# Performance work log

Hardware: AMD Instinct MI355X
Metric: run time of the kernel (lower is better)

## Reference

```python
import jax, jax.numpy as jnp
import numpy as np

V, E, H, B, T = 50257, 300, 512, 4, 512  # vocab, embed(300 fixed), hid_size, batch, max_seq_len


def setup_inputs() -> dict:
    key = jax.random.key(0)
    ks = jax.random.split(key, 12)
    n = lambda k, shp, s: jax.random.normal(k, shp, dtype=jnp.float32) * s
    return {
        "tokens": jax.random.randint(ks[0], (B, T), 0, V),
        "emb_table": n(ks[1], (V, E), 0.02),      # frozen pretrained embedding
        # forward-direction LstmCellWithProjection params (cell_size == hidden_size == H)
        "W_ih_f": n(ks[2], (E, 4 * H), 0.05),     # input_linearity (no bias)
        "W_hh_f": n(ks[3], (H, 4 * H), 0.05),     # state_linearity weight
        "b_f": jnp.zeros((4 * H,), jnp.float32),  # state_linearity bias
        "W_proj_f": n(ks[4], (H, H), 0.05),       # state_projection (no bias)
        # backward direction
        "W_ih_b": n(ks[5], (E, 4 * H), 0.05),
        "W_hh_b": n(ks[6], (H, 4 * H), 0.05),
        "b_b": jnp.zeros((4 * H,), jnp.float32),
        "W_proj_b": n(ks[7], (H, H), 0.05),
        # final vocab projection nn.Linear(H, V)
        "W_lin": n(ks[8], (H, V), 0.02),
        "b_lin": jnp.zeros((V,), jnp.float32),
    }


def _lstm_proj_scan(x, W_ih, W_hh, b, W_proj):
    """ElmoLstm's LstmCellWithProjection over time. x: [B,T,E] -> [B,T,H]."""
    xp = jnp.einsum("bte,eg->btg", x, W_ih)  # precompute input projections [B,T,4H]

    def step(carry, xt):  # xt: [B,4H]
        h, c = carry
        p = xt + h @ W_hh + b
        i = jax.nn.sigmoid(p[:, :H])
        f = jax.nn.sigmoid(p[:, H:2 * H])
        g = jnp.tanh(p[:, 2 * H:3 * H])
        o = jax.nn.sigmoid(p[:, 3 * H:])
        c2 = i * g + f * c
        h2 = (o * jnp.tanh(c2)) @ W_proj  # projected hidden state
        return (h2, c2), h2

    init = (jnp.zeros((x.shape[0], H), x.dtype), jnp.zeros((x.shape[0], H), x.dtype))
    _, hs = jax.lax.scan(step, init, jnp.swapaxes(xp, 0, 1))  # [T,B,H]
    return jnp.swapaxes(hs, 0, 1)  # [B,T,H]


def reference(tokens, emb_table, W_ih_f, W_hh_f, b_f, W_proj_f,
              W_ih_b, W_hh_b, b_b, W_proj_b, W_lin, b_lin):
    x = emb_table[tokens]  # embedding gather [B,T,E]
    fwd = _lstm_proj_scan(x, W_ih_f, W_hh_f, b_f, W_proj_f)
    bwd = _lstm_proj_scan(x[:, ::-1], W_ih_b, W_hh_b, b_b, W_proj_b)[:, ::-1]
    # num_layers == 1 -> enc is (1,B,T,2H); fwd half / bwd half each through shared Linear
    logits_fwd = (fwd @ W_lin + b_lin).reshape(-1, V)  # [B*T, V]
    logits_bwd = (bwd @ W_lin + b_lin).reshape(-1, V)
    return jnp.concatenate([logits_fwd, logits_bwd], axis=0)  # [2*B*T, V]
```

## Files before the change

kernel.cpp:

```cpp
#include <hip/hip_runtime.h>
#include <hip/hip_bf16.h>

typedef unsigned short u16;
typedef unsigned int u32;
typedef unsigned long long u64;
typedef short bf16x8 __attribute__((ext_vector_type(8)));
typedef float f32x4 __attribute__((ext_vector_type(4)));

#define AS1C(p) ((const __attribute__((address_space(1))) void*)(p))
#define AS3(p)  ((__attribute__((address_space(3))) void*)(p))

__device__ __forceinline__ u16 f2bf(float f) {
    union { float f; unsigned u; } v; v.f = f;
    unsigned x = v.u;
    unsigned r = (x + 0x7FFFu + ((x >> 16) & 1u)) >> 16;
    return (u16)r;
}

__global__ void zero_init(u64* htag) {
    for (int i = threadIdx.x; i < 2 * 2 * 4 * 256; i += 256) htag[i] = 0ull;
}

__global__ void gather_emb(const int* __restrict__ tokens, const float* __restrict__ emb,
                           u16* __restrict__ xemb) {
    int row = blockIdx.x;
    int tok = tokens[row];
    const float* src = emb + (size_t)tok * 300;
    u16* dst = xemb + (size_t)row * 320;
    int c = threadIdx.x;
    if (c < 320) dst[c] = (c < 300) ? f2bf(src[c]) : (u16)0;
    c += 256;
    if (c < 320) dst[c] = (c < 300) ? f2bf(src[c]) : (u16)0;
}

__global__ void transpose_cvt(const float* __restrict__ in, u16* __restrict__ out,
                              int R, int C, int outR, int ldO) {
    __shared__ float tile[32][33];
    int c0 = blockIdx.x * 32, r0 = blockIdx.y * 32;
    int tx = threadIdx.x & 31, ty = threadIdx.x >> 5;
#pragma unroll
    for (int yy = 0; yy < 4; ++yy) {
        int r = r0 + ty + yy * 8, cc = c0 + tx;
        tile[ty + yy * 8][tx] = (r < R && cc < C) ? in[(size_t)r * C + cc] : 0.f;
    }
    __syncthreads();
#pragma unroll
    for (int yy = 0; yy < 4; ++yy) {
        int c = c0 + ty + yy * 8, r = r0 + tx;
        if (c < outR && r < ldO) out[(size_t)c * ldO + r] = f2bf(tile[tx][ty + yy * 8]);
    }
}

__global__ void cvt_flat(const float* __restrict__ in, u16* __restrict__ out, int n) {
    for (int i = blockIdx.x * 256 + threadIdx.x; i < n; i += gridDim.x * 256)
        out[i] = f2bf(in[i]);
}

__global__ __launch_bounds__(256) void gemm_bf16(
    const u16* __restrict__ A, const u16* __restrict__ BT,
    float* __restrict__ Cf, u16* __restrict__ Cb,
    const float* __restrict__ bias,
    int M, int Nreal, int K, int ldA, int ldB, int ldC,
    int arev, int orev, int orow_base)
{
    __shared__ char As[8192];
    __shared__ char Bs[8192];
    const int tid = threadIdx.x;
    const int lane = tid & 63;
    const int wid = tid >> 6;
    const int wr = wid >> 1, wc = wid & 1;
    const int m0 = blockIdx.y * 128;
    const int n0 = blockIdx.x * 128;

    f32x4 zero4 = {0.f, 0.f, 0.f, 0.f};
    f32x4 acc[4][4];
#pragma unroll
    for (int i = 0; i < 4; ++i)
#pragma unroll
        for (int j = 0; j < 4; ++j) acc[i][j] = zero4;

    const int kIters = K >> 5;
    const int l15 = lane & 15, kg = lane >> 4;

    const int srow0 = wid * 32 + (lane >> 2);
    const int srow1 = srow0 + 16;
    const int c0 = (lane & 3) ^ (srow0 & 3);
    const int c1 = (lane & 3) ^ (srow1 & 3);
    int ar0 = m0 + srow0, ar1 = m0 + srow1;
    if (arev) {
        ar0 = (ar0 & ~511) | (511 - (ar0 & 511));
        ar1 = (ar1 & ~511) | (511 - (ar1 & 511));
    }
    const u16* ga0 = A + (size_t)ar0 * ldA + c0 * 8;
    const u16* ga1 = A + (size_t)ar1 * ldA + c1 * 8;
    const u16* gb0 = BT + (size_t)(n0 + srow0) * ldB + c0 * 8;
    const u16* gb1 = BT + (size_t)(n0 + srow1) * ldB + c1 * 8;
    char* ldsA0 = As + wid * 2048;
    char* ldsA1 = As + wid * 2048 + 1024;
    char* ldsB0 = Bs + wid * 2048;
    char* ldsB1 = Bs + wid * 2048 + 1024;

    for (int kt = 0; kt < kIters; ++kt) {
        const int k0 = kt * 32;
        __builtin_amdgcn_global_load_lds(AS1C(ga0 + k0), AS3(ldsA0), 16, 0, 0);
        __builtin_amdgcn_global_load_lds(AS1C(ga1 + k0), AS3(ldsA1), 16, 0, 0);
        __builtin_amdgcn_global_load_lds(AS1C(gb0 + k0), AS3(ldsB0), 16, 0, 0);
        __builtin_amdgcn_global_load_lds(AS1C(gb1 + k0), AS3(ldsB1), 16, 0, 0);
        __syncthreads();

        bf16x8 af[4], bfr[4];
#pragma unroll
        for (int mt = 0; mt < 4; ++mt) {
            int r = wr * 64 + mt * 16 + l15;
            af[mt] = *(const bf16x8*)(As + r * 64 + ((kg ^ (r & 3)) * 16));
        }
#pragma unroll
        for (int nt = 0; nt < 4; ++nt) {
            int r = wc * 64 + nt * 16 + l15;
            bfr[nt] = *(const bf16x8*)(Bs + r * 64 + ((kg ^ (r & 3)) * 16));
        }
#pragma unroll
        for (int mt = 0; mt < 4; ++mt)
#pragma unroll
            for (int nt = 0; nt < 4; ++nt)
                acc[mt][nt] = __builtin_amdgcn_mfma_f32_16x16x32_bf16(af[mt], bfr[nt], acc[mt][nt], 0, 0, 0);
        __syncthreads();
    }

#pragma unroll
    for (int nt = 0; nt < 4; ++nt) {
        int col = n0 + wc * 64 + nt * 16 + l15;
        float bv = (bias != nullptr && col < Nreal) ? bias[col] : 0.f;
#pragma unroll
        for (int mt = 0; mt < 4; ++mt) {
#pragma unroll
            for (int j = 0; j < 4; ++j) {
                int m = m0 + wr * 64 + mt * 16 + kg * 4 + j;
                int om = orev ? ((m & ~511) | (511 - (m & 511))) : m;
                om += orow_base;
                if (col < Nreal) {
                    float v = acc[mt][nt][j] + bv;
                    if (Cf) Cf[(size_t)om * ldC + col] = v;
                    else    Cb[(size_t)om * ldC + col] = f2bf(v);
                }
            }
        }
    }
}

__global__ __launch_bounds__(256) void lstm_rec(
    const float* __restrict__ Wc_f, const float* __restrict__ Wc_b,
    const float* __restrict__ xp_f, const float* __restrict__ xp_b,
    u64* __restrict__ htag,
    u16* __restrict__ hpre_f, u16* __restrict__ hpre_b)
{
    __shared__ u16 hlds[4][520];
    __shared__ float gsum[4][4][16];
    __shared__ float cbuf[4][16];
    const int tid = threadIdx.x;
    const int dir = blockIdx.x >> 5;
    const int blk = blockIdx.x & 31;
    const int lane = tid & 63;
    const int wid = tid >> 6;
    const int l15 = lane & 15;
    const int kg = lane >> 4;

    const float* wcsrc = dir ? Wc_b : Wc_f;
    const float* xp    = dir ? xp_b : xp_f;
    u16* hpre          = dir ? hpre_b : hpre_f;
    u64* ht            = htag + (size_t)dir * 2 * 4 * 256;

    bf16x8 wcf[16];
#pragma unroll
    for (int ks = 0; ks < 16; ++ks) {
        bf16x8 w;
#pragma unroll
        for (int e = 0; e < 8; ++e) {
            int k = ks * 32 + kg * 8 + e;
            w[e] = (short)f2bf(wcsrc[(size_t)k * 2048 + wid * 512 + blk * 16 + l15]);
        }
        wcf[ks] = w;
    }
    if (tid < 64) cbuf[tid >> 4][tid & 15] = 0.f;
    __syncthreads();

    const bf16x8 zero8 = {0, 0, 0, 0, 0, 0, 0, 0};

    for (int t = 0; t < 512; ++t) {
        float xpv0 = 0.f, xpv1 = 0.f, xpv2 = 0.f, xpv3 = 0.f;
        const int b = tid >> 4, hu = tid & 15;
        if (tid < 64) {
            const float* xr = xp + ((size_t)(b * 512 + t)) * 2048 + blk * 16 + hu;
            xpv0 = xr[0]; xpv1 = xr[512]; xpv2 = xr[1024]; xpv3 = xr[1536];
        }
        {
            const u64* src = ht + (size_t)(t & 1) * 4 * 256;
            const u32 target = (u32)t;
            u64 w0, w1, w2, w3;
            for (;;) {
                w0 = __hip_atomic_load(&src[0 * 256 + tid], __ATOMIC_RELAXED, __HIP_MEMORY_SCOPE_AGENT);
                w1 = __hip_atomic_load(&src[1 * 256 + tid], __ATOMIC_RELAXED, __HIP_MEMORY_SCOPE_AGENT);
                w2 = __hip_atomic_load(&src[2 * 256 + tid], __ATOMIC_RELAXED, __HIP_MEMORY_SCOPE_AGENT);
                w3 = __hip_atomic_load(&src[3 * 256 + tid], __ATOMIC_RELAXED, __HIP_MEMORY_SCOPE_AGENT);
                if (((u32)(w0 >> 32) == target) & ((u32)(w1 >> 32) == target) &
                    ((u32)(w2 >> 32) == target) & ((u32)(w3 >> 32) == target)) break;
                __builtin_amdgcn_s_sleep(1);
            }
            asm volatile("" ::: "memory");
            *(u32*)&hlds[0][tid * 2] = (u32)w0;
            *(u32*)&hlds[1][tid * 2] = (u32)w1;
            *(u32*)&hlds[2][tid * 2] = (u32)w2;
            *(u32*)&hlds[3][tid * 2] = (u32)w3;
        }
        __syncthreads();

        f32x4 acc0 = {0.f, 0.f, 0.f, 0.f}, acc1 = {0.f, 0.f, 0.f, 0.f};
#pragma unroll
        for (int ks = 0; ks < 16; ++ks) {
            bf16x8 a = zero8;
            if (l15 < 4) a = *(const bf16x8*)&hlds[l15][ks * 32 + kg * 8];
            if (ks & 1) acc1 = __builtin_amdgcn_mfma_f32_16x16x32_bf16(a, wcf[ks], acc1, 0, 0, 0);
            else        acc0 = __builtin_amdgcn_mfma_f32_16x16x32_bf16(a, wcf[ks], acc0, 0, 0, 0);
        }
        f32x4 accs = acc0 + acc1;
        if (lane < 16) {
#pragma unroll
            for (int j = 0; j < 4; ++j) gsum[wid][j][lane] = accs[j];
        }
        __syncthreads();

        if (tid < 64) {
            float pi = xpv0 + gsum[0][b][hu];
            float pf = xpv1 + gsum[1][b][hu];
            float pg = xpv2 + gsum[2][b][hu];
            float po = xpv3 + gsum[3][b][hu];
            float iv = 1.f / (1.f + expf(-pi));
            float fv = 1.f / (1.f + expf(-pf));
            float gv = tanhf(pg);
            float ov = 1.f / (1.f + expf(-po));
            float c2 = iv * gv + fv * cbuf[b][hu];
            cbuf[b][hu] = c2;
            u16 hpb = f2bf(ov * tanhf(c2));
            hpre[(size_t)(b * 512 + t) * 512 + blk * 16 + hu] = hpb;
            unsigned v = hpb;
            unsigned nb = (unsigned)__shfl_down((int)v, 1);
            if ((tid & 1) == 0) {
                u32 packed = v | (nb << 16);
                u64 val = ((u64)(u32)(t + 1) << 32) | (u64)packed;
                size_t idx = (size_t)(((t + 1) & 1) * 4 + b) * 256 + blk * 8 + (hu >> 1);
                __hip_atomic_store(&ht[idx], val, __ATOMIC_RELAXED, __HIP_MEMORY_SCOPE_AGENT);
            }
        }
    }
}

extern "C" void kernel_launch(void* const* d_in, const int* in_sizes, int n_in,
                              void* d_out, int out_size, void* d_ws, size_t ws_size,
                              hipStream_t stream) {
    const int*   tokens   = (const int*)d_in[0];
    const float* emb      = (const float*)d_in[1];
    const float* W_ih_f   = (const float*)d_in[2];
    const float* W_hh_f   = (const float*)d_in[3];
    const float* b_f      = (const float*)d_in[4];
    const float* W_proj_f = (const float*)d_in[5];
    const float* W_ih_b   = (const float*)d_in[6];
    const float* W_hh_b   = (const float*)d_in[7];
    const float* b_b      = (const float*)d_in[8];
    const float* W_proj_b = (const float*)d_in[9];
    const float* W_lin    = (const float*)d_in[10];
    const float* b_lin    = (const float*)d_in[11];
    float* out = (float*)d_out;

    char* ws = (char*)d_ws;
    size_t off = 0;
    auto alloc = [&](size_t bytes) -> char* {
        char* p = ws + off;
        off = (off + bytes + 255) & ~(size_t)255;
        return p;
    };
    u16* xemb     = (u16*)alloc(2048 * 320 * 2);
    u16* WT_ihf   = (u16*)alloc(2048 * 320 * 2);
    u16* WT_ihb   = (u16*)alloc(2048 * 320 * 2);
    u16* WT_hhf   = (u16*)alloc(2048 * 512 * 2);
    u16* WT_hhb   = (u16*)alloc(2048 * 512 * 2);
    u16* WprojTf  = (u16*)alloc(512 * 512 * 2);
    u16* WprojTb  = (u16*)alloc(512 * 512 * 2);
    u16* WprojAf  = (u16*)alloc(512 * 512 * 2);
    u16* WprojAb  = (u16*)alloc(512 * 512 * 2);
    u16* WT_lin   = (u16*)alloc((size_t)50304 * 512 * 2);
    float* xpf    = (float*)alloc((size_t)2048 * 2048 * 4);
    float* xpb    = (float*)alloc((size_t)2048 * 2048 * 4);
    float* Wc32f  = (float*)alloc((size_t)512 * 2048 * 4);
    float* Wc32b  = (float*)alloc((size_t)512 * 2048 * 4);
    u16* hpref    = (u16*)alloc((size_t)2048 * 512 * 2);
    u16* hpreb    = (u16*)alloc((size_t)2048 * 512 * 2);
    u16* hall     = (u16*)alloc((size_t)4096 * 512 * 2);
    u64* htag     = (u64*)alloc((size_t)2 * 2 * 4 * 256 * 8);

    zero_init<<<1, 256, 0, stream>>>(htag);
    gather_emb<<<2048, 256, 0, stream>>>(tokens, emb, xemb);

    transpose_cvt<<<dim3(64, 10), 256, 0, stream>>>(W_ih_f, WT_ihf, 300, 2048, 2048, 320);
    transpose_cvt<<<dim3(64, 10), 256, 0, stream>>>(W_ih_b, WT_ihb, 300, 2048, 2048, 320);
    transpose_cvt<<<dim3(64, 16), 256, 0, stream>>>(W_hh_f, WT_hhf, 512, 2048, 2048, 512);
    transpose_cvt<<<dim3(64, 16), 256, 0, stream>>>(W_hh_b, WT_hhb, 512, 2048, 2048, 512);
    transpose_cvt<<<dim3(16, 16), 256, 0, stream>>>(W_proj_f, WprojTf, 512, 512, 512, 512);
    transpose_cvt<<<dim3(16, 16), 256, 0, stream>>>(W_proj_b, WprojTb, 512, 512, 512, 512);
    transpose_cvt<<<dim3(1572, 16), 256, 0, stream>>>(W_lin, WT_lin, 512, 50257, 50304, 512);
    cvt_flat<<<512, 256, 0, stream>>>(W_proj_f, WprojAf, 512 * 512);
    cvt_flat<<<512, 256, 0, stream>>>(W_proj_b, WprojAb, 512 * 512);

    gemm_bf16<<<dim3(16, 16), 256, 0, stream>>>(xemb, WT_ihf, xpf, nullptr, b_f,
                                                2048, 2048, 320, 320, 320, 2048, 0, 0, 0);
    gemm_bf16<<<dim3(16, 16), 256, 0, stream>>>(xemb, WT_ihb, xpb, nullptr, b_b,
                                                2048, 2048, 320, 320, 320, 2048, 1, 0, 0);
    gemm_bf16<<<dim3(16, 4), 256, 0, stream>>>(WprojAf, WT_hhf, Wc32f, nullptr, nullptr,
                                               512, 2048, 512, 512, 512, 2048, 0, 0, 0);
    gemm_bf16<<<dim3(16, 4), 256, 0, stream>>>(WprojAb, WT_hhb, Wc32b, nullptr, nullptr,
                                               512, 2048, 512, 512, 512, 2048, 0, 0, 0);

    lstm_rec<<<64, 256, 0, stream>>>(Wc32f, Wc32b, xpf, xpb, htag, hpref, hpreb);

    gemm_bf16<<<dim3(4, 16), 256, 0, stream>>>(hpref, WprojTf, nullptr, hall, nullptr,
                                               2048, 512, 512, 512, 512, 512, 0, 0, 0);
    gemm_bf16<<<dim3(4, 16), 256, 0, stream>>>(hpreb, WprojTb, nullptr, hall, nullptr,
                                               2048, 512, 512, 512, 512, 512, 0, 1, 2048);
    gemm_bf16<<<dim3(393, 32), 256, 0, stream>>>(hall, WT_lin, out, nullptr, b_lin,
                                                 4096, 50257, 512, 512, 512, 50257, 0, 0, 0);
}
```

Baseline: 1.859 ms.

## Merge prep kernels, batch GEMMs, and overlap W_lin transpose with LSTM recurrence

After: 1.793 ms. 3.6% less time.

```diff
diff --git a/kernel.cpp b/kernel.cpp
--- a/kernel.cpp
+++ b/kernel.cpp
@@ -17,26 +17,10 @@
     return (u16)r;
 }
 
-__global__ void zero_init(u64* htag) {
-    for (int i = threadIdx.x; i < 2 * 2 * 4 * 256; i += 256) htag[i] = 0ull;
-}
-
-__global__ void gather_emb(const int* __restrict__ tokens, const float* __restrict__ emb,
-                           u16* __restrict__ xemb) {
-    int row = blockIdx.x;
-    int tok = tokens[row];
-    const float* src = emb + (size_t)tok * 300;
-    u16* dst = xemb + (size_t)row * 320;
-    int c = threadIdx.x;
-    if (c < 320) dst[c] = (c < 300) ? f2bf(src[c]) : (u16)0;
-    c += 256;
-    if (c < 320) dst[c] = (c < 300) ? f2bf(src[c]) : (u16)0;
-}
-
-__global__ void transpose_cvt(const float* __restrict__ in, u16* __restrict__ out,
-                              int R, int C, int outR, int ldO) {
-    __shared__ float tile[32][33];
-    int c0 = blockIdx.x * 32, r0 = blockIdx.y * 32;
+__device__ __forceinline__ void tpose_dev(float (*tile)[33],
+        const float* __restrict__ in, u16* __restrict__ out,
+        int R, int C, int outR, int ldO, int bx, int by) {
+    int c0 = bx * 32, r0 = by * 32;
     int tx = threadIdx.x & 31, ty = threadIdx.x >> 5;
 #pragma unroll
     for (int yy = 0; yy < 4; ++yy) {
@@ -51,18 +35,56 @@
     }
 }
 
-__global__ void cvt_flat(const float* __restrict__ in, u16* __restrict__ out, int n) {
-    for (int i = blockIdx.x * 256 + threadIdx.x; i < n; i += gridDim.x * 256)
-        out[i] = f2bf(in[i]);
-}
-
-__global__ __launch_bounds__(256) void gemm_bf16(
-    const u16* __restrict__ A, const u16* __restrict__ BT,
-    float* __restrict__ Cf, u16* __restrict__ Cb,
-    const float* __restrict__ bias,
-    int M, int Nreal, int K, int ldA, int ldB, int ldC,
-    int arev, int orev, int orow_base)
+__global__ __launch_bounds__(256) void prep(
+    const int* __restrict__ tokens, const float* __restrict__ emb, u16* __restrict__ xemb,
+    const float* __restrict__ W_ih_f, u16* __restrict__ WT_ihf,
+    const float* __restrict__ W_ih_b, u16* __restrict__ WT_ihb,
+    const float* __restrict__ W_hh_f, u16* __restrict__ WT_hhf,
+    const float* __restrict__ W_hh_b, u16* __restrict__ WT_hhb,
+    const float* __restrict__ W_proj_f, u16* __restrict__ WprojTf,
+    const float* __restrict__ W_proj_b, u16* __restrict__ WprojTb,
+    u16* __restrict__ WprojAf, u16* __restrict__ WprojAb,
+    u64* __restrict__ htag)
 {
+    __shared__ float tile[32][33];
+    int bid = blockIdx.x;
+    int tid = threadIdx.x;
+    if (bid < 2048) {
+        int tok = tokens[bid];
+        const float* src = emb + (size_t)tok * 300;
+        u16* dst = xemb + (size_t)bid * 320;
+        int c = tid;
+        if (c < 320) dst[c] = (c < 300) ? f2bf(src[c]) : (u16)0;
+        c += 256;
+        if (c < 320) dst[c] = (c < 300) ? f2bf(src[c]) : (u16)0;
+        return;
+    }
+    bid -= 2048;
+    if (bid < 640)  { tpose_dev(tile, W_ih_f, WT_ihf, 300, 2048, 2048, 320, bid % 64, bid / 64); return; }
+    bid -= 640;
+    if (bid < 640)  { tpose_dev(tile, W_ih_b, WT_ihb, 300, 2048, 2048, 320, bid % 64, bid / 64); return; }
+    bid -= 640;
+    if (bid < 1024) { tpose_dev(tile, W_hh_f, WT_hhf, 512, 2048, 2048, 512, bid % 64, bid / 64); return; }
+    bid -= 1024;
+    if (bid < 1024) { tpose_dev(tile, W_hh_b, WT_hhb, 512, 2048, 2048, 512, bid % 64, bid / 64); return; }
+    bid -= 1024;
+    if (bid < 256)  { tpose_dev(tile, W_proj_f, WprojTf, 512, 512, 512, 512, bid % 16, bid / 16); return; }
+    bid -= 256;
+    if (bid < 256)  { tpose_dev(tile, W_proj_b, WprojTb, 512, 512, 512, 512, bid % 16, bid / 16); return; }
+    bid -= 256;
+    if (bid < 512)  { int i = bid * 512 + tid; WprojAf[i] = f2bf(W_proj_f[i]); WprojAf[i + 256] = f2bf(W_proj_f[i + 256]); return; }
+    bid -= 512;
+    if (bid < 512)  { int i = bid * 512 + tid; WprojAb[i] = f2bf(W_proj_b[i]); WprojAb[i + 256] = f2bf(W_proj_b[i + 256]); return; }
+    bid -= 512;
+    for (int i = tid; i < 2 * 2 * 4 * 256; i += 256) htag[i] = 0ull;
+}
+
+struct GemmJob {
+    const u16* A; const u16* BT; float* Cf; u16* Cb; const float* bias;
+    int M, Nreal, K, ldA, ldB, ldC, arev, orev, orow_base;
+};
+
+__device__ __forceinline__ void gemm_body(const GemmJob& j) {
     __shared__ char As[8192];
     __shared__ char Bs[8192];
     const int tid = threadIdx.x;
@@ -77,9 +99,9 @@
 #pragma unroll
     for (int i = 0; i < 4; ++i)
 #pragma unroll
-        for (int j = 0; j < 4; ++j) acc[i][j] = zero4;
-
-    const int kIters = K >> 5;
+        for (int jx = 0; jx < 4; ++jx) acc[i][jx] = zero4;
+
+    const int kIters = j.K >> 5;
     const int l15 = lane & 15, kg = lane >> 4;
 
     const int srow0 = wid * 32 + (lane >> 2);
@@ -87,14 +109,14 @@
     const int c0 = (lane & 3) ^ (srow0 & 3);
     const int c1 = (lane & 3) ^ (srow1 & 3);
     int ar0 = m0 + srow0, ar1 = m0 + srow1;
-    if (arev) {
+    if (j.arev) {
         ar0 = (ar0 & ~511) | (511 - (ar0 & 511));
         ar1 = (ar1 & ~511) | (511 - (ar1 & 511));
     }
-    const u16* ga0 = A + (size_t)ar0 * ldA + c0 * 8;
-    const u16* ga1 = A + (size_t)ar1 * ldA + c1 * 8;
-    const u16* gb0 = BT + (size_t)(n0 + srow0) * ldB + c0 * 8;
-    const u16* gb1 = BT + (size_t)(n0 + srow1) * ldB + c1 * 8;
+    const u16* ga0 = j.A + (size_t)ar0 * j.ldA + c0 * 8;
+    const u16* ga1 = j.A + (size_t)ar1 * j.ldA + c1 * 8;
+    const u16* gb0 = j.BT + (size_t)(n0 + srow0) * j.ldB + c0 * 8;
+    const u16* gb1 = j.BT + (size_t)(n0 + srow1) * j.ldB + c1 * 8;
     char* ldsA0 = As + wid * 2048;
     char* ldsA1 = As + wid * 2048 + 1024;
     char* ldsB0 = Bs + wid * 2048;
@@ -130,33 +152,54 @@
 #pragma unroll
     for (int nt = 0; nt < 4; ++nt) {
         int col = n0 + wc * 64 + nt * 16 + l15;
-        float bv = (bias != nullptr && col < Nreal) ? bias[col] : 0.f;
+        float bv = (j.bias != nullptr && col < j.Nreal) ? j.bias[col] : 0.f;
 #pragma unroll
         for (int mt = 0; mt < 4; ++mt) {
 #pragma unroll
-            for (int j = 0; j < 4; ++j) {
-                int m = m0 + wr * 64 + mt * 16 + kg * 4 + j;
-                int om = orev ? ((m & ~511) | (511 - (m & 511))) : m;
-                om += orow_base;
-                if (col < Nreal) {
-                    float v = acc[mt][nt][j] + bv;
-                    if (Cf) Cf[(size_t)om * ldC + col] = v;
-                    else    Cb[(size_t)om * ldC + col] = f2bf(v);
+            for (int jx = 0; jx < 4; ++jx) {
+                int m = m0 + wr * 64 + mt * 16 + kg * 4 + jx;
+                int om = j.orev ? ((m & ~511) | (511 - (m & 511))) : m;
+                om += j.orow_base;
+                if (col < j.Nreal) {
+                    float v = acc[mt][nt][jx] + bv;
+                    if (j.Cf) j.Cf[(size_t)om * j.ldC + col] = v;
+                    else      j.Cb[(size_t)om * j.ldC + col] = f2bf(v);
                 }
             }
         }
     }
 }
 
-__global__ __launch_bounds__(256) void lstm_rec(
+__global__ __launch_bounds__(256) void gemm_multi4(GemmJob j0, GemmJob j1, GemmJob j2, GemmJob j3) {
+    GemmJob j = (blockIdx.z == 0) ? j0 : (blockIdx.z == 1) ? j1 : (blockIdx.z == 2) ? j2 : j3;
+    if ((int)blockIdx.y * 128 >= j.M) return;
+    gemm_body(j);
+}
+__global__ __launch_bounds__(256) void gemm_multi2(GemmJob j0, GemmJob j1) {
+    GemmJob j = blockIdx.z ? j1 : j0;
+    gemm_body(j);
+}
+__global__ __launch_bounds__(256) void gemm_one(GemmJob j0) { gemm_body(j0); }
+
+__global__ __launch_bounds__(256) void lstm_fused(
     const float* __restrict__ Wc_f, const float* __restrict__ Wc_b,
     const float* __restrict__ xp_f, const float* __restrict__ xp_b,
     u64* __restrict__ htag,
-    u16* __restrict__ hpre_f, u16* __restrict__ hpre_b)
+    u16* __restrict__ hpre_f, u16* __restrict__ hpre_b,
+    const float* __restrict__ W_lin, u16* __restrict__ WT_lin)
 {
+    __shared__ float tile[32][33];
     __shared__ u16 hlds[4][520];
     __shared__ float gsum[4][4][16];
     __shared__ float cbuf[4][16];
+
+    if (blockIdx.x >= 64) {
+        int job = blockIdx.x - 64;
+        tpose_dev(tile, W_lin, WT_lin, 512, 50257, 50304, 512, job % 1572, job / 1572);
+        return;
+    }
+    __builtin_amdgcn_s_setprio(1);
+
     const int tid = threadIdx.x;
     const int dir = blockIdx.x >> 5;
     const int blk = blockIdx.x & 31;
@@ -185,23 +228,32 @@
     __syncthreads();
 
     const bf16x8 zero8 = {0, 0, 0, 0, 0, 0, 0, 0};
+    const int b = tid >> 4, hu = tid & 15;
 
     for (int t = 0; t < 512; ++t) {
         float xpv0 = 0.f, xpv1 = 0.f, xpv2 = 0.f, xpv3 = 0.f;
-        const int b = tid >> 4, hu = tid & 15;
         if (tid < 64) {
             const float* xr = xp + ((size_t)(b * 512 + t)) * 2048 + blk * 16 + hu;
             xpv0 = xr[0]; xpv1 = xr[512]; xpv2 = xr[1024]; xpv3 = xr[1536];
         }
         {
             const u64* src = ht + (size_t)(t & 1) * 4 * 256;
+            const u64* p0 = src + tid;
+            const u64* p1 = src + 256 + tid;
+            const u64* p2 = src + 512 + tid;
+            const u64* p3 = src + 768 + tid;
             const u32 target = (u32)t;
             u64 w0, w1, w2, w3;
             for (;;) {
-                w0 = __hip_atomic_load(&src[0 * 256 + tid], __ATOMIC_RELAXED, __HIP_MEMORY_SCOPE_AGENT);
-                w1 = __hip_atomic_load(&src[1 * 256 + tid], __ATOMIC_RELAXED, __HIP_MEMORY_SCOPE_AGENT);
-                w2 = __hip_atomic_load(&src[2 * 256 + tid], __ATOMIC_RELAXED, __HIP_MEMORY_SCOPE_AGENT);
-                w3 = __hip_atomic_load(&src[3 * 256 + tid], __ATOMIC_RELAXED, __HIP_MEMORY_SCOPE_AGENT);
+                asm volatile(
+                    "global_load_dwordx2 %0, %4, off sc0 sc1\n\t"
+                    "global_load_dwordx2 %1, %5, off sc0 sc1\n\t"
+                    "global_load_dwordx2 %2, %6, off sc0 sc1\n\t"
+                    "global_load_dwordx2 %3, %7, off sc0 sc1\n\t"
+                    "s_waitcnt vmcnt(0)"
+                    : "=&v"(w0), "=&v"(w1), "=&v"(w2), "=&v"(w3)
+                    : "v"(p0), "v"(p1), "v"(p2), "v"(p3)
+                    : "memory");
                 if (((u32)(w0 >> 32) == target) & ((u32)(w1 >> 32) == target) &
                     ((u32)(w2 >> 32) == target) & ((u32)(w3 >> 32) == target)) break;
                 __builtin_amdgcn_s_sleep(1);
@@ -214,18 +266,22 @@
         }
         __syncthreads();
 
-        f32x4 acc0 = {0.f, 0.f, 0.f, 0.f}, acc1 = {0.f, 0.f, 0.f, 0.f};
+        f32x4 a0 = {0,0,0,0}, a1 = {0,0,0,0}, a2 = {0,0,0,0}, a3 = {0,0,0,0};
 #pragma unroll
         for (int ks = 0; ks < 16; ++ks) {
             bf16x8 a = zero8;
             if (l15 < 4) a = *(const bf16x8*)&hlds[l15][ks * 32 + kg * 8];
-            if (ks & 1) acc1 = __builtin_amdgcn_mfma_f32_16x16x32_bf16(a, wcf[ks], acc1, 0, 0, 0);
-            else        acc0 = __builtin_amdgcn_mfma_f32_16x16x32_bf16(a, wcf[ks], acc0, 0, 0, 0);
-        }
-        f32x4 accs = acc0 + acc1;
+            switch (ks & 3) {
+                case 0: a0 = __builtin_amdgcn_mfma_f32_16x16x32_bf16(a, wcf[ks], a0, 0, 0, 0); break;
+                case 1: a1 = __builtin_amdgcn_mfma_f32_16x16x32_bf16(a, wcf[ks], a1, 0, 0, 0); break;
+                case 2: a2 = __builtin_amdgcn_mfma_f32_16x16x32_bf16(a, wcf[ks], a2, 0, 0, 0); break;
+                default: a3 = __builtin_amdgcn_mfma_f32_16x16x32_bf16(a, wcf[ks], a3, 0, 0, 0); break;
+            }
+        }
+        f32x4 accs = (a0 + a1) + (a2 + a3);
         if (lane < 16) {
 #pragma unroll
-            for (int j = 0; j < 4; ++j) gsum[wid][j][lane] = accs[j];
+            for (int jx = 0; jx < 4; ++jx) gsum[wid][jx][lane] = accs[jx];
         }
         __syncthreads();
 
@@ -241,7 +297,6 @@
             float c2 = iv * gv + fv * cbuf[b][hu];
             cbuf[b][hu] = c2;
             u16 hpb = f2bf(ov * tanhf(c2));
-            hpre[(size_t)(b * 512 + t) * 512 + blk * 16 + hu] = hpb;
             unsigned v = hpb;
             unsigned nb = (unsigned)__shfl_down((int)v, 1);
             if ((tid & 1) == 0) {
@@ -250,6 +305,7 @@
                 size_t idx = (size_t)(((t + 1) & 1) * 4 + b) * 256 + blk * 8 + (hu >> 1);
                 __hip_atomic_store(&ht[idx], val, __ATOMIC_RELAXED, __HIP_MEMORY_SCOPE_AGENT);
             }
+            hpre[(size_t)(b * 512 + t) * 512 + blk * 16 + hu] = hpb;
         }
     }
 }
@@ -297,34 +353,25 @@
     u16* hall     = (u16*)alloc((size_t)4096 * 512 * 2);
     u64* htag     = (u64*)alloc((size_t)2 * 2 * 4 * 256 * 8);
 
-    zero_init<<<1, 256, 0, stream>>>(htag);
-    gather_emb<<<2048, 256, 0, stream>>>(tokens, emb, xemb);
-
-    transpose_cvt<<<dim3(64, 10), 256, 0, stream>>>(W_ih_f, WT_ihf, 300, 2048, 2048, 320);
-    transpose_cvt<<<dim3(64, 10), 256, 0, stream>>>(W_ih_b, WT_ihb, 300, 2048, 2048, 320);
-    transpose_cvt<<<dim3(64, 16), 256, 0, stream>>>(W_hh_f, WT_hhf, 512, 2048, 2048, 512);
-    transpose_cvt<<<dim3(64, 16), 256, 0, stream>>>(W_hh_b, WT_hhb, 512, 2048, 2048, 512);
-    transpose_cvt<<<dim3(16, 16), 256, 0, stream>>>(W_proj_f, WprojTf, 512, 512, 512, 512);
-    transpose_cvt<<<dim3(16, 16), 256, 0, stream>>>(W_proj_b, WprojTb, 512, 512, 512, 512);
-    transpose_cvt<<<dim3(1572, 16), 256, 0, stream>>>(W_lin, WT_lin, 512, 50257, 50304, 512);
-    cvt_flat<<<512, 256, 0, stream>>>(W_proj_f, WprojAf, 512 * 512);
-    cvt_flat<<<512, 256, 0, stream>>>(W_proj_b, WprojAb, 512 * 512);
-
-    gemm_bf16<<<dim3(16, 16), 256, 0, stream>>>(xemb, WT_ihf, xpf, nullptr, b_f,
-                                                2048, 2048, 320, 320, 320, 2048, 0, 0, 0);
-    gemm_bf16<<<dim3(16, 16), 256, 0, stream>>>(xemb, WT_ihb, xpb, nullptr, b_b,
-                                                2048, 2048, 320, 320, 320, 2048, 1, 0, 0);
-    gemm_bf16<<<dim3(16, 4), 256, 0, stream>>>(WprojAf, WT_hhf, Wc32f, nullptr, nullptr,
-                                               512, 2048, 512, 512, 512, 2048, 0, 0, 0);
-    gemm_bf16<<<dim3(16, 4), 256, 0, stream>>>(WprojAb, WT_hhb, Wc32b, nullptr, nullptr,
-                                               512, 2048, 512, 512, 512, 2048, 0, 0, 0);
-
-    lstm_rec<<<64, 256, 0, stream>>>(Wc32f, Wc32b, xpf, xpb, htag, hpref, hpreb);
-
-    gemm_bf16<<<dim3(4, 16), 256, 0, stream>>>(hpref, WprojTf, nullptr, hall, nullptr,
-                                               2048, 512, 512, 512, 512, 512, 0, 0, 0);
-    gemm_bf16<<<dim3(4, 16), 256, 0, stream>>>(hpreb, WprojTb, nullptr, hall, nullptr,
-                                               2048, 512, 512, 512, 512, 512, 0, 1, 2048);
-    gemm_bf16<<<dim3(393, 32), 256, 0, stream>>>(hall, WT_lin, out, nullptr, b_lin,
-                                                 4096, 50257, 512, 512, 512, 50257, 0, 0, 0);
-}
+    prep<<<6913, 256, 0, stream>>>(tokens, emb, xemb,
+                                   W_ih_f, WT_ihf, W_ih_b, WT_ihb,
+                                   W_hh_f, WT_hhf, W_hh_b, WT_hhb,
+                                   W_proj_f, WprojTf, W_proj_b, WprojTb,
+                                   WprojAf, WprojAb, htag);
+
+    GemmJob jxf = {xemb, WT_ihf, xpf, nullptr, b_f, 2048, 2048, 320, 320, 320, 2048, 0, 0, 0};
+    GemmJob jxb = {xemb, WT_ihb, xpb, nullptr, b_b, 2048, 2048, 320, 320, 320, 2048, 1, 0, 0};
+    GemmJob jwf = {WprojAf, WT_hhf, Wc32f, nullptr, nullptr, 512, 2048, 512, 512, 512, 2048, 0, 0, 0};
+    GemmJob jwb = {WprojAb, WT_hhb, Wc32b, nullptr, nullptr, 512, 2048, 512, 512, 512, 2048, 0, 0, 0};
+    gemm_multi4<<<dim3(16, 16, 4), 256, 0, stream>>>(jxf, jxb, jwf, jwb);
+
+    lstm_fused<<<64 + 1572 * 16, 256, 0, stream>>>(Wc32f, Wc32b, xpf, xpb, htag,
+                                                   hpref, hpreb, W_lin, WT_lin);
+
+    GemmJob jpf = {hpref, WprojTf, nullptr, hall, nullptr, 2048, 512, 512, 512, 512, 512, 0, 0, 0};
+    GemmJob jpb = {hpreb, WprojTb, nullptr, hall, nullptr, 2048, 512, 512, 512, 512, 512, 0, 1, 2048};
+    gemm_multi2<<<dim3(4, 16, 2), 256, 0, stream>>>(jpf, jpb);
+
+    GemmJob jl = {hall, WT_lin, out, nullptr, b_lin, 4096, 50257, 512, 512, 512, 50257, 0, 0, 0};
+    gemm_one<<<dim3(393, 32), 256, 0, stream>>>(jl);
+}
```
